# Kernel optimization log

Hardware: AMD Instinct MI355X
Metric: run time of the kernel (lower is better)

Reference implementation:

```python
import jax, jax.numpy as jnp
import numpy as np

N_NODES = 20000
N_EDGES = 640000
HID = 256
IN_F, IN_SIZE = 6, 6
OUT_F, FH = 6, 3
EDGE_DIM = 8
T_DIM, S_DIM = 4, 6
N_LAYERS = 5


def setup_inputs() -> dict:
    key = jax.random.key(0)
    ks = jax.random.split(key, 32)
    g = lambda i, shape, scale=0.05: jax.random.normal(ks[i], shape, dtype=jnp.float32) * scale
    inp = {
        "x": jax.random.normal(ks[0], (N_NODES, IN_F, IN_SIZE), dtype=jnp.float32),
        "edge_index": jax.random.randint(ks[1], (2, N_EDGES), 0, N_NODES, dtype=jnp.int32),
        "edge_attr": jax.random.normal(ks[2], (N_EDGES, EDGE_DIM), dtype=jnp.float32),
        "t": jax.random.normal(ks[3], (N_NODES, T_DIM), dtype=jnp.float32),
        "s": jax.random.normal(ks[4], (N_NODES, S_DIM), dtype=jnp.float32),
        # embedder
        "W_emb": g(5, (IN_F * IN_SIZE, HID)), "b_emb": jnp.zeros((HID,), jnp.float32),
        # spatio-temporal encoder: t/s linear embeds + fusion over concat(x, te, se)
        "W_t": g(6, (T_DIM, HID)), "b_t": jnp.zeros((HID,), jnp.float32),
        "W_s": g(7, (S_DIM, HID)), "b_s": jnp.zeros((HID,), jnp.float32),
        "W_f": g(8, (3 * HID, HID)), "b_f": jnp.zeros((HID,), jnp.float32),
        # layernorm
        "ln_g": jnp.ones((HID,), jnp.float32), "ln_b": jnp.zeros((HID,), jnp.float32),
        # 5 TransformerConv layers (heads=1): query/key/value/edge/skip linears
        "Wq": g(9, (N_LAYERS, HID, HID)), "bq": jnp.zeros((N_LAYERS, HID), jnp.float32),
        "Wk": g(10, (N_LAYERS, HID, HID)), "bk": jnp.zeros((N_LAYERS, HID), jnp.float32),
        "Wv": g(11, (N_LAYERS, HID, HID)), "bv": jnp.zeros((N_LAYERS, HID), jnp.float32),
        "We": g(12, (N_LAYERS, EDGE_DIM, HID)), "be": jnp.zeros((N_LAYERS, HID), jnp.float32),
        "Wskip": g(13, (N_LAYERS, HID, HID)), "bskip": jnp.zeros((N_LAYERS, HID), jnp.float32),
        # decoder
        "W_dec": g(14, (HID, OUT_F * FH)), "b_dec": jnp.zeros((OUT_F * FH,), jnp.float32),
    }
    return inp


def _layernorm(x, g, b, eps=1e-5):
    mu = jnp.mean(x, axis=-1, keepdims=True)
    var = jnp.mean((x - mu) ** 2, axis=-1, keepdims=True)
    return (x - mu) * jax.lax.rsqrt(var + eps) * g + b


def _transformer_conv(x, src, dst, edge_attr, Wq, bq, Wk, bk, Wv, bv, We, be, Wskip, bskip):
    n = x.shape[0]
    d = x.shape[1]
    q = x @ Wq + bq                      # [n, d]
    k = x @ Wk + bk
    v = x @ Wv + bv
    e = edge_attr @ We + be              # [E, d]
    kj = k[src] + e                      # gather + edge fuse [E, d]
    vj = v[src] + e
    alpha = jnp.sum(q[dst] * kj, axis=-1) / jnp.sqrt(jnp.float32(d))  # [E]
    # segment softmax over incoming edges of each destination node
    m = jax.ops.segment_max(alpha, dst, num_segments=n)
    a = jnp.exp(alpha - m[dst])
    denom = jax.ops.segment_sum(a, dst, num_segments=n)
    w = a / (denom[dst] + 1e-16)
    out = jax.ops.segment_sum(vj * w[:, None], dst, num_segments=n)  # [n, d]
    return out + x @ Wskip + bskip       # root/skip connection


def reference(x, edge_index, edge_attr, t, s,
              W_emb, b_emb, W_t, b_t, W_s, b_s, W_f, b_f, ln_g, ln_b,
              Wq, bq, Wk, bk, Wv, bv, We, be, Wskip, bskip, W_dec, b_dec):
    n = x.shape[0]
    h = x.reshape(n, -1) @ W_emb + b_emb
    te = t @ W_t + b_t
    se = s @ W_s + b_s
    h = jnp.concatenate([h, te, se], axis=-1) @ W_f + b_f   # spatio-temporal fuse
    h = jax.nn.relu(_layernorm(h, ln_g, ln_b))
    src, dst = edge_index[0], edge_index[1]
    for i in range(N_LAYERS):
        h = jax.nn.relu(_transformer_conv(h, src, dst, edge_attr,
                                          Wq[i], bq[i], Wk[i], bk[i], Wv[i], bv[i],
                                          We[i], be[i], Wskip[i], bskip[i]))
    out = h @ W_dec + b_dec
    return out.reshape(n, OUT_F, FH)
```

## Files before the change

kernel.cpp:

```cpp
#include <hip/hip_runtime.h>
#include <hip/hip_fp8.h>
#include <math.h>

#define NN 20000
#define NPAD 20096
#define NE 640000
#define NOUT 1152
#define GSS 272
#define KVB 512
#define CAP 80
#define SCQ 0.09016994f
#define ISCL 8.8057e-5f
#define TIDX(r,k) ((((r)>>4)*4096) + (((k)>>3)*128) + (((r)&15)*8) + ((k)&7))

typedef _Float16 f16;
typedef f16 f16x8 __attribute__((ext_vector_type(8)));
typedef f16 f16x4 __attribute__((ext_vector_type(4)));
typedef f16 h2    __attribute__((ext_vector_type(2)));
typedef float f32x4 __attribute__((ext_vector_type(4)));
typedef float f32x2 __attribute__((ext_vector_type(2)));

static __device__ __forceinline__ float fdot2(h2 a, h2 b, float c) {
#if __has_builtin(__builtin_amdgcn_fdot2)
  return __builtin_amdgcn_fdot2(a, b, c, false);
#else
  return c + (float)a[0]*(float)b[0] + (float)a[1]*(float)b[1];
#endif
}

static __device__ __forceinline__ float fast_exp2(float x) {
#if __has_builtin(__builtin_amdgcn_exp2f)
  return __builtin_amdgcn_exp2f(x);
#else
  return exp2f(x);
#endif
}

static __device__ __forceinline__ int sdot4(unsigned a, unsigned b, int c) {
#if __has_builtin(__builtin_amdgcn_sdot4)
  return __builtin_amdgcn_sdot4((int)a, (int)b, c, false);
#else
  int r = c;
  #pragma unroll
  for (int i = 0; i < 4; i++) {
    int ai = ((int)((a >> (8*i)) & 255) ^ 128) - 128;
    int bi = ((int)((b >> (8*i)) & 255) ^ 128) - 128;
    r += ai*bi;
  }
  return r;
#endif
}

static __device__ __forceinline__ unsigned pack_i8x4(float a, float b, float c, float d) {
  int i0 = (int)rintf(a), i1 = (int)rintf(b), i2 = (int)rintf(c), i3 = (int)rintf(d);
  i0 = max(-127, min(127, i0)); i1 = max(-127, min(127, i1));
  i2 = max(-127, min(127, i2)); i3 = max(-127, min(127, i3));
  return (unsigned)(i0 & 255) | ((unsigned)(i1 & 255) << 8)
       | ((unsigned)(i2 & 255) << 16) | ((unsigned)(i3 & 255) << 24);
}

static __device__ __forceinline__ unsigned pack_fp8x4(float a, float b, float c, float d) {
#if __has_builtin(__builtin_amdgcn_cvt_pk_fp8_f32)
  int r = __builtin_amdgcn_cvt_pk_fp8_f32(a, b, 0, false);
  r = __builtin_amdgcn_cvt_pk_fp8_f32(c, d, r, true);
  return (unsigned)r;
#else
  __hip_fp8_e4m3 w(a), x2(b), y(c), z(d);
  return (unsigned)w.__x | ((unsigned)x2.__x<<8) | ((unsigned)y.__x<<16) | ((unsigned)z.__x<<24);
#endif
}

template<bool HI>
static __device__ __forceinline__ f32x2 unpack_fp8x2(unsigned v) {
#if __has_builtin(__builtin_amdgcn_cvt_pk_f32_fp8)
  return __builtin_amdgcn_cvt_pk_f32_fp8((int)v, HI);
#else
  unsigned s = HI ? (v >> 16) : (v & 0xffff);
  __hip_fp8_e4m3 a, b; a.__x = (unsigned char)(s & 0xff); b.__x = (unsigned char)(s >> 8);
  return (f32x2){ (float)a, (float)b };
#endif
}

__global__ __launch_bounds__(256) void k_prep_all(
    const float* __restrict__ W_emb, const float* __restrict__ W_t,
    const float* __restrict__ W_s,   const float* __restrict__ W_f,
    const float* __restrict__ b_emb, const float* __restrict__ b_t,
    const float* __restrict__ b_s,   const float* __restrict__ b_f,
    const float* __restrict__ Wq, const float* __restrict__ Wk,
    const float* __restrict__ Wv, const float* __restrict__ Wsk,
    const float* __restrict__ We, const float* __restrict__ be,
    const float* __restrict__ bq, const float* __restrict__ bk,
    const float* __restrict__ bv, const float* __restrict__ bsk,
    f16* __restrict__ Wch, float* __restrict__ bc,
    f16* __restrict__ WT, float* __restrict__ b_all,
    f16* __restrict__ hA, f16* __restrict__ hB)
{
  __shared__ float smem[64*65];
  int b = blockIdx.x;
  int tid = threadIdx.x;

  if (b < 47) {
    int r = b, c = tid;
    if (r < 36) {
      float a = 0.f;
      for (int m = 0; m < 256; m++) a += W_emb[r*256+m] * W_f[m*256+c];
      Wch[r*256+c] = (f16)a;
    } else if (r < 40) {
      int rr = r - 36; float a = 0.f;
      for (int m = 0; m < 256; m++) a += W_t[rr*256+m] * W_f[(256+m)*256+c];
      Wch[r*256+c] = (f16)a;
    } else if (r < 46) {
      int rr = r - 40; float a = 0.f;
      for (int m = 0; m < 256; m++) a += W_s[rr*256+m] * W_f[(512+m)*256+c];
      Wch[r*256+c] = (f16)a;
    } else {
      float a = b_f[c];
      for (int m = 0; m < 256; m++) a += b_emb[m]*W_f[m*256+c];
      for (int m = 0; m < 256; m++) a += b_t[m]*W_f[(256+m)*256+c];
      for (int m = 0; m < 256; m++) a += b_s[m]*W_f[(512+m)*256+c];
      bc[c] = a;
    }
  } else if (b < 367) {
    float (*lds)[65] = (float(*)[65])smem;
    int bb = b - 47;
    int nt = bb & 3, kt = (bb >> 2) & 3, mat = (bb >> 4) & 3, L = bb >> 6;
    const float* src = (mat == 0 ? Wq : mat == 1 ? Wk : mat == 2 ? Wv : Wsk) + (size_t)L*65536;
    int k0 = kt*64, n0 = nt*64;
    int c = tid & 63, r4 = tid >> 6;
    #pragma unroll
    for (int rr = 0; rr < 16; rr++) {
      int row = rr*4 + r4;
      lds[row][c] = src[(size_t)(k0 + row)*256 + n0 + c];
    }
    __syncthreads();
    f16* dst = WT + (size_t)L*294912;
    int nl = tid & 63, kb2 = tid >> 6;
    int ng = mat*256 + n0 + nl;
    #pragma unroll
    for (int half = 0; half < 2; half++) {
      int kb = kb2 + half*4;
      f16x8 v;
      #pragma unroll
      for (int e = 0; e < 8; e++) v[e] = (f16)lds[kb*8 + e][nl];
      *(f16x8*)(dst + TIDX(ng, k0 + kb*8)) = v;
    }
  } else if (b < 412) {
    float* vec = smem;
    int bb = b - 367;
    int L = bb / 9;
    int t = bb % 9;
    vec[tid] = (t < 8) ? We[(size_t)L*2048 + t*256 + tid] : be[(size_t)L*256 + tid];
    __syncthreads();
    int wave = tid >> 6, lane = tid & 63;
    for (int k = wave; k < 256; k += 4) {
      f32x4 wq = *(const f32x4*)(Wq + (size_t)L*65536 + (size_t)k*256 + lane*4);
      f32x4 vv = *(const f32x4*)(vec + lane*4);
      float d = wq[0]*vv[0] + wq[1]*vv[1] + wq[2]*vv[2] + wq[3]*vv[3];
      #pragma unroll
      for (int o = 32; o; o >>= 1) d += __shfl_xor(d, o, 64);
      if (lane == 0) WT[(size_t)L*294912 + TIDX(1024 + t, k)] = (f16)d;
    }
  } else if (b < 417) {
    int L = b - 412;
    for (int c = tid; c < NOUT; c += 256) {
      float v;
      if (c < 256)       v = bq [L*256+c];
      else if (c < 512)  v = bk [L*256+(c-256)];
      else if (c < 768)  v = bv [L*256+(c-512)];
      else if (c < 1024) v = bsk[L*256+(c-768)];
      else if (c < 1032) {
        int t = c-1024; float a = 0.f;
        for (int m = 0; m < 256; m++) a += bq[L*256+m]*We[(size_t)L*2048 + t*256 + m];
        v = a;
      } else if (c == 1032) {
        float a = 0.f;
        for (int m = 0; m < 256; m++) a += bq[L*256+m]*be[L*256+m];
        v = a;
      } else v = 0.f;
      b_all[(size_t)L*NOUT + c] = v;
    }
  } else {
    f16* p = (b == 417 ? hA : hB) + (size_t)NN*256;
    f16x8 z = {};
    for (int i = tid; i < (NPAD-NN)*256/8; i += 256)
      *(f16x8*)(p + (size_t)i*8) = z;
  }
}

__global__ void k_scatter(const int* __restrict__ ei, const float* __restrict__ eattr,
                          int* cnt, int* __restrict__ src_s, f16* __restrict__ eaperm)
{
  int e = blockIdx.x*256 + threadIdx.x;
  if (e < NE) {
    int d = ei[NE + e];
    int pos = atomicAdd(&cnt[d], 1);
    int slot = d*CAP + pos;
    src_s[slot] = ei[e];
    f32x4 a0 = *(const f32x4*)(eattr + (size_t)e*8);
    f32x4 a1 = *(const f32x4*)(eattr + (size_t)e*8 + 4);
    f16x8 ea = { (f16)a0[0],(f16)a0[1],(f16)a0[2],(f16)a0[3],
                 (f16)a1[0],(f16)a1[1],(f16)a1[2],(f16)a1[3] };
    *(f16x8*)(eaperm + (size_t)slot*8) = ea;
  }
}

__global__ __launch_bounds__(256) void k_encoder(
    const float* __restrict__ x, const float* __restrict__ t, const float* __restrict__ s,
    const f16* __restrict__ Wch, const float* __restrict__ bc,
    const float* __restrict__ lng, const float* __restrict__ lnb,
    f16* __restrict__ h)
{
  __shared__ f16 Wcs[46*256];
  __shared__ float xin[16][48];
  __shared__ float bcs[256], lgs[256], lbs[256];
  int tid = threadIdx.x;
  int u0 = blockIdx.x * 16;
  for (int i = tid; i < 46*128; i += 256)
    ((unsigned int*)Wcs)[i] = ((const unsigned int*)Wch)[i];
  bcs[tid] = bc[tid]; lgs[tid] = lng[tid]; lbs[tid] = lnb[tid];
  for (int i = tid; i < 576; i += 256) xin[i/36][i%36] = x[(size_t)u0*36 + i];
  if (tid < 64) xin[tid>>2][36 + (tid&3)] = t[(size_t)u0*4 + tid];
  if (tid < 96) xin[tid/6][40 + tid%6] = s[(size_t)u0*6 + tid];
  __syncthreads();
  int node = tid >> 4, cg = tid & 15;
  int u = u0 + node;
  float acc[16];
  #pragma unroll
  for (int j = 0; j < 16; j++) acc[j] = bcs[cg*16+j];
  for (int r = 0; r < 46; r++) {
    float xv = xin[node][r];
    const h2* wr = (const h2*)(Wcs + r*256 + cg*16);
    #pragma unroll
    for (int j2 = 0; j2 < 8; j2++) {
      h2 w2 = wr[j2];
      acc[j2*2]   += xv * (float)w2[0];
      acc[j2*2+1] += xv * (float)w2[1];
    }
  }
  float sm = 0.f, sq = 0.f;
  #pragma unroll
  for (int j = 0; j < 16; j++) { sm += acc[j]; sq += acc[j]*acc[j]; }
  #pragma unroll
  for (int o = 1; o < 16; o <<= 1) { sm += __shfl_xor(sm, o, 64); sq += __shfl_xor(sq, o, 64); }
  float mu  = sm * (1.f/256.f);
  float var = sq * (1.f/256.f) - mu*mu;
  float rin = rsqrtf(var + 1e-5f);
  f16x8 o0, o1;
  #pragma unroll
  for (int j = 0; j < 8; j++) {
    int c = cg*16 + j;
    float v = (acc[j]-mu)*rin*lgs[c] + lbs[c];
    o0[j] = (f16)fmaxf(v, 0.f);
  }
  #pragma unroll
  for (int j = 0; j < 8; j++) {
    int c = cg*16 + 8 + j;
    float v = (acc[8+j]-mu)*rin*lgs[c] + lbs[c];
    o1[j] = (f16)fmaxf(v, 0.f);
  }
  *(f16x8*)(h + TIDX(u, cg*16))   = o0;
  *(f16x8*)(h + TIDX(u, cg*16+8)) = o1;
}

__global__ __launch_bounds__(256) void k_gemm(
    const f16* __restrict__ A, const f16* __restrict__ BT,
    const float* __restrict__ bias,
    unsigned char* __restrict__ qt8, unsigned char* __restrict__ kvt,
    f16* __restrict__ gsk)
{
  const int NWG = (NPAD/128)*9;
  const int Q = NWG >> 3, R = NWG & 7;
  int bid = blockIdx.x;
  int xcd = bid & 7, jj = bid >> 3;
  int wg = (xcd < R ? xcd*(Q+1) : R*(Q+1) + (xcd-R)*Q) + jj;
  int bmt = wg / 9, bnt = wg - bmt*9;

  int tid = threadIdx.x;
  int wave = tid >> 6, lane = tid & 63;
  int wm = wave >> 1, wn = wave & 1;
  int bm = bmt*128 + wm*64;
  int bn = bnt*128 + wn*64;
  int lr = lane & 15;
  int kg = lane >> 4;
  f32x4 acc[4][4];
  #pragma unroll
  for (int i = 0; i < 4; i++)
    #pragma unroll
    for (int j = 0; j < 4; j++) acc[i][j] = (f32x4){0.f,0.f,0.f,0.f};

  const f16* Ab = A  + (size_t)(bm >> 4)*4096 + kg*128 + lr*8;
  const f16* Bb = BT + (size_t)(bn >> 4)*4096 + kg*128 + lr*8;
  #pragma unroll
  for (int k0 = 0; k0 < 256; k0 += 32) {
    f16x8 af[4], bf[4];
    #pragma unroll
    for (int i = 0; i < 4; i++) af[i] = *(const f16x8*)(Ab + i*4096 + k0*16);
    #pragma unroll
    for (int j = 0; j < 4; j++) bf[j] = *(const f16x8*)(Bb + j*4096 + k0*16);
    #pragma unroll
    for (int i = 0; i < 4; i++)
      #pragma unroll
      for (int j = 0; j < 4; j++)
        acc[i][j] = __builtin_amdgcn_mfma_f32_16x16x32_f16(bf[j], af[i], acc[i][j], 0, 0, 0);
  }

  #pragma unroll
  for (int j = 0; j < 4; j++) {
    int cb0 = bn + j*16;
    if (cb0 >= 1040) continue;
    int colq = cb0 + kg*4;
    f32x4 bv = *(const f32x4*)(bias + colq);
    #pragma unroll
    for (int i = 0; i < 4; i++) {
      int row = bm + i*16 + lr;
      float v0 = acc[i][j][0]+bv[0], v1 = acc[i][j][1]+bv[1];
      float v2 = acc[i][j][2]+bv[2], v3 = acc[i][j][3]+bv[3];
      if (cb0 < 256) {
        *(unsigned*)(qt8 + (size_t)row*256 + colq) = pack_i8x4(v0*32.f, v1*32.f, v2*32.f, v3*32.f);
      } else if (cb0 < 512) {
        *(unsigned*)(kvt + (size_t)row*KVB + (colq-256)) = pack_i8x4(v0*32.f, v1*32.f, v2*32.f, v3*32.f);
      } else if (cb0 < 768) {
        *(unsigned*)(kvt + (size_t)row*KVB + 256 + (colq-512)) = pack_fp8x4(v0, v1, v2, v3);
      } else if (cb0 < 1024) {
        f16x4 st = { (f16)v0, (f16)v1, (f16)v2, (f16)v3 };
        *(f16x4*)(gsk + (size_t)row*GSS + (colq-768)) = st;
      } else {
        f16x4 st = { (f16)(v0*SCQ), (f16)(v1*SCQ), (f16)(v2*SCQ), (f16)(v3*SCQ) };
        *(f16x4*)(gsk + (size_t)row*GSS + 256 + (colq-1024)) = st;
      }
    }
  }
}

__global__ __launch_bounds__(256) void k_alpha(
    const unsigned char* __restrict__ qt8, const unsigned char* __restrict__ kvt,
    const f16* __restrict__ gsk, const f16* __restrict__ eaperm,
    const int* __restrict__ cnt, const int* __restrict__ src_s,
    float* __restrict__ wbuf)
{
  int wid = threadIdx.x >> 6, lane = threadIdx.x & 63;
  int u = __builtin_amdgcn_readfirstlane(blockIdx.x*4 + wid);
  int deg = cnt[u];
  const uint4* qp = (const uint4*)(qt8 + (size_t)u*256);
  uint4 q[16];
  #pragma unroll
  for (int c = 0; c < 16; c++) q[c] = qp[c];
  const f16* gb = gsk + (size_t)u*GSS;
  f16x8 qe8 = *(const f16x8*)(gb + 256);
  float qbv = (float)gb[264];
  size_t ub = (size_t)u*CAP;
  for (int i = lane; i < deg; i += 64) {
    int sn = src_s[ub + i];
    const uint4* kp = (const uint4*)(kvt + (size_t)sn*KVB);
    int di = 0;
    #pragma unroll
    for (int c = 0; c < 16; c++) {
      uint4 kw = kp[c];
      di = sdot4(kw.x, q[c].x, di);
      di = sdot4(kw.y, q[c].y, di);
      di = sdot4(kw.z, q[c].z, di);
      di = sdot4(kw.w, q[c].w, di);
    }
    f16x8 ea = *(const f16x8*)(eaperm + (ub + i)*8);
    float edot = 0.f;
    edot = fdot2((h2){ea[0],ea[1]}, (h2){qe8[0],qe8[1]}, edot);
    edot = fdot2((h2){ea[2],ea[3]}, (h2){qe8[2],qe8[3]}, edot);
    edot = fdot2((h2){ea[4],ea[5]}, (h2){qe8[4],qe8[5]}, edot);
    edot = fdot2((h2){ea[6],ea[7]}, (h2){qe8[6],qe8[7]}, edot);
    wbuf[ub + i] = fast_exp2((float)di*ISCL + edot + qbv);
  }
}

__global__ __launch_bounds__(256) void k_attn2(
    const unsigned char* __restrict__ kvt, const f16* __restrict__ gsk,
    const f16* __restrict__ eaperm,
    const float* __restrict__ WeL, const float* __restrict__ beL,
    const int* __restrict__ cnt, const int* __restrict__ src_s,
    const float* __restrict__ wbuf, f16* __restrict__ hout)
{
  int wid  = threadIdx.x >> 6;
  int lane = threadIdx.x & 63;
  int grp  = lane >> 4;
  int gl   = lane & 15;
  int u = blockIdx.x*4 + wid;
  int deg = cnt[u];

  float ssum = 0.f;
  float av[16];
  float ae[8];
  #pragma unroll
  for (int j = 0; j < 16; j++) av[j] = 0.f;
  #pragma unroll
  for (int j = 0; j < 8; j++) ae[j] = 0.f;

  size_t ub = (size_t)u*CAP;
  #pragma unroll 2
  for (int i = grp; i < deg; i += 4) {
    int sn = src_s[ub + i];
    uint4 vw = *(const uint4*)(kvt + (size_t)sn*KVB + 256 + gl*16);
    f16x8 ea = *(const f16x8*)(eaperm + (ub + i)*8);
    float w = wbuf[ub + i];
    ssum += w;
    f32x2 p;
    p = unpack_fp8x2<false>(vw.x); av[0]  += w*p[0]; av[1]  += w*p[1];
    p = unpack_fp8x2<true >(vw.x); av[2]  += w*p[0]; av[3]  += w*p[1];
    p = unpack_fp8x2<false>(vw.y); av[4]  += w*p[0]; av[5]  += w*p[1];
    p = unpack_fp8x2<true >(vw.y); av[6]  += w*p[0]; av[7]  += w*p[1];
    p = unpack_fp8x2<false>(vw.z); av[8]  += w*p[0]; av[9]  += w*p[1];
    p = unpack_fp8x2<true >(vw.z); av[10] += w*p[0]; av[11] += w*p[1];
    p = unpack_fp8x2<false>(vw.w); av[12] += w*p[0]; av[13] += w*p[1];
    p = unpack_fp8x2<true >(vw.w); av[14] += w*p[0]; av[15] += w*p[1];
    #pragma unroll
    for (int j = 0; j < 8; j++) ae[j] += w*(float)ea[j];
  }

  #pragma unroll
  for (int j = 0; j < 16; j++) {
    av[j] += __shfl_xor(av[j], 16, 64);
    av[j] += __shfl_xor(av[j], 32, 64);
  }
  #pragma unroll
  for (int j = 0; j < 8; j++) {
    ae[j] += __shfl_xor(ae[j], 16, 64);
    ae[j] += __shfl_xor(ae[j], 32, 64);
  }
  ssum += __shfl_xor(ssum, 16, 64);
  ssum += __shfl_xor(ssum, 32, 64);

  float inv = 1.f/(ssum + 1e-16f);
  const f16* gb = gsk + (size_t)u*GSS;
  int cb = gl*16 + grp*4;
  f16 res[4];
  #pragma unroll
  for (int t = 0; t < 4; t++) {
    int c = cb + t;
    float o = av[grp*4+t];
    #pragma unroll
    for (int e = 0; e < 8; e++) o += ae[e]*WeL[e*256 + c];
    o += ssum*beL[c];
    o = o*inv + (float)gb[c];
    res[t] = (f16)fmaxf(o, 0.f);
  }
  f16x4 outp = { res[0], res[1], res[2], res[3] };
  *(f16x4*)(hout + TIDX(u, cb)) = outp;
}

__global__ __launch_bounds__(256) void k_decoder(
    const f16* __restrict__ h, const float* __restrict__ Wd,
    const float* __restrict__ bd, float* __restrict__ out)
{
  int n0 = blockIdx.x*32;
  __shared__ float hs[32*256];
  int tid = threadIdx.x;
  for (int j = tid; j < 32*32; j += 256) {
    int node = j >> 5, c8 = (j & 31)*8;
    f16x8 v = *(const f16x8*)(h + TIDX(n0 + node, c8));
    float* dst = &hs[node*256 + c8];
    #pragma unroll
    for (int e = 0; e < 8; e++) dst[e] = (float)v[e];
  }
  __syncthreads();
  for (int o = tid; o < 32*18; o += 256) {
    int ln = o/18, col = o - ln*18;
    int node = n0 + ln;
    float acc = bd[col];
    const float* hr = &hs[ln*256];
    #pragma unroll 4
    for (int k4 = 0; k4 < 64; k4++) {
      f32x4 hv = *(const f32x4*)(hr + k4*4);
      acc += hv[0]*Wd[(k4*4+0)*18+col] + hv[1]*Wd[(k4*4+1)*18+col]
           + hv[2]*Wd[(k4*4+2)*18+col] + hv[3]*Wd[(k4*4+3)*18+col];
    }
    out[(size_t)node*18 + col] = acc;
  }
}

extern "C" void kernel_launch(void* const* d_in, const int* in_sizes, int n_in,
                              void* d_out, int out_size, void* d_ws, size_t ws_size,
                              hipStream_t stream)
{
  const float* x     = (const float*)d_in[0];
  const int*   ei    = (const int*)  d_in[1];
  const float* eattr = (const float*)d_in[2];
  const float* t     = (const float*)d_in[3];
  const float* s     = (const float*)d_in[4];
  const float* W_emb = (const float*)d_in[5];
  const float* b_emb = (const float*)d_in[6];
  const float* W_t   = (const float*)d_in[7];
  const float* b_t   = (const float*)d_in[8];
  const float* W_s   = (const float*)d_in[9];
  const float* b_s   = (const float*)d_in[10];
  const float* W_f   = (const float*)d_in[11];
  const float* b_f   = (const float*)d_in[12];
  const float* ln_g  = (const float*)d_in[13];
  const float* ln_b  = (const float*)d_in[14];
  const float* Wq    = (const float*)d_in[15];
  const float* bq    = (const float*)d_in[16];
  const float* Wk    = (const float*)d_in[17];
  const float* bk    = (const float*)d_in[18];
  const float* Wv    = (const float*)d_in[19];
  const float* bv    = (const float*)d_in[20];
  const float* We    = (const float*)d_in[21];
  const float* be    = (const float*)d_in[22];
  const float* Wsk   = (const float*)d_in[23];
  const float* bsk   = (const float*)d_in[24];
  const float* W_dec = (const float*)d_in[25];
  const float* b_dec = (const float*)d_in[26];

  float* wsf = (float*)d_ws;
  size_t off = 0;
  float* bc    = wsf + off; off += 256;
  float* b_all = wsf + off; off += (size_t)5*NOUT;
  f16*   Wch   = (f16*)(wsf + off); off += (size_t)46*256/2;
  f16*   WT    = (f16*)(wsf + off); off += (size_t)5*294912/2;
  unsigned char* qt8 = (unsigned char*)(wsf + off); off += (size_t)NPAD*256/4;
  unsigned char* kvt = (unsigned char*)(wsf + off); off += (size_t)NPAD*KVB/4;
  f16*   gsk   = (f16*)(wsf + off); off += (size_t)NPAD*GSS/2;
  f16*   hA    = (f16*)(wsf + off); off += (size_t)NPAD*256/2;
  f16*   hB    = (f16*)(wsf + off); off += (size_t)NPAD*256/2;
  f16*   eaperm= (f16*)(wsf + off); off += (size_t)NN*CAP*8/2;
  int*   src_s = (int*)(wsf + off); off += (size_t)NN*CAP;
  float* wbuf  = wsf + off; off += (size_t)NN*CAP;
  int*   cnt   = (int*)(wsf + off); off += NN;

  (void)hipMemsetAsync(cnt, 0, NN*sizeof(int), stream);
  k_prep_all<<<419, 256, 0, stream>>>(W_emb, W_t, W_s, W_f, b_emb, b_t, b_s, b_f,
                                      Wq, Wk, Wv, Wsk, We, be, bq, bk, bv, bsk,
                                      Wch, bc, WT, b_all, hA, hB);
  k_scatter <<<(NE+255)/256, 256, 0, stream>>>(ei, eattr, cnt, src_s, eaperm);

  k_encoder <<<NN/16, 256, 0, stream>>>(x, t, s, Wch, bc, ln_g, ln_b, hA);

  f16* hin = hA;
  f16* hot = hB;
  for (int L = 0; L < 5; L++) {
    k_gemm<<<(NPAD/128)*9, 256, 0, stream>>>(hin, WT + (size_t)L*294912,
                                             b_all + (size_t)L*NOUT, qt8, kvt, gsk);
    k_alpha<<<NN/4, 256, 0, stream>>>(qt8, kvt, gsk, eaperm, cnt, src_s, wbuf);
    k_attn2<<<NN/4, 256, 0, stream>>>(kvt, gsk, eaperm, We + (size_t)L*2048,
                                      be + (size_t)L*256, cnt, src_s, wbuf, hot);
    f16* tmp = hin; hin = hot; hot = tmp;
  }
  k_decoder<<<NN/32, 256, 0, stream>>>(hin, W_dec, b_dec, (float*)d_out);
}
```

Before: 581.9 us.

## Pack per-edge records and move edge-attr reduction into alpha kernel

Merges the separate edge-attr, source-index and weight arrays into one 32-byte record per edge slot. The alpha kernel now also reduces the softmax denominator and weighted edge attributes per node into a small stats buffer. The aggregation kernel therefore only gathers value rows, with each lane owning 4 columns and walking all edges serially instead of splitting edges across 4 lane groups. This cuts scattered loads and shuffle reductions, but it serialises the edge loop per wave and widens the per-edge record footprint.

```diff
diff --git a/kernel.cpp b/kernel.cpp
--- a/kernel.cpp
+++ b/kernel.cpp
@@ -9,6 +9,7 @@
 #define GSS 272
 #define KVB 512
 #define CAP 80
+#define RECB 32
 #define SCQ 0.09016994f
 #define ISCL 8.8057e-5f
 #define TIDX(r,k) ((((r)>>4)*4096) + (((k)>>3)*128) + (((r)&15)*8) + ((k)&7))
@@ -188,19 +189,19 @@
 }
 
 __global__ void k_scatter(const int* __restrict__ ei, const float* __restrict__ eattr,
-                          int* cnt, int* __restrict__ src_s, f16* __restrict__ eaperm)
+                          int* cnt, char* __restrict__ rec)
 {
   int e = blockIdx.x*256 + threadIdx.x;
   if (e < NE) {
     int d = ei[NE + e];
     int pos = atomicAdd(&cnt[d], 1);
-    int slot = d*CAP + pos;
-    src_s[slot] = ei[e];
+    char* rp = rec + (size_t)(d*CAP + pos)*RECB;
     f32x4 a0 = *(const f32x4*)(eattr + (size_t)e*8);
     f32x4 a1 = *(const f32x4*)(eattr + (size_t)e*8 + 4);
     f16x8 ea = { (f16)a0[0],(f16)a0[1],(f16)a0[2],(f16)a0[3],
                  (f16)a1[0],(f16)a1[1],(f16)a1[2],(f16)a1[3] };
-    *(f16x8*)(eaperm + (size_t)slot*8) = ea;
+    *(f16x8*)rp = ea;
+    *(int*)(rp + 16) = ei[e];
   }
 }
 
@@ -334,9 +335,8 @@
 
 __global__ __launch_bounds__(256) void k_alpha(
     const unsigned char* __restrict__ qt8, const unsigned char* __restrict__ kvt,
-    const f16* __restrict__ gsk, const f16* __restrict__ eaperm,
-    const int* __restrict__ cnt, const int* __restrict__ src_s,
-    float* __restrict__ wbuf)
+    const f16* __restrict__ gsk, char* __restrict__ rec,
+    const int* __restrict__ cnt, float* __restrict__ stats)
 {
   int wid = threadIdx.x >> 6, lane = threadIdx.x & 63;
   int u = __builtin_amdgcn_readfirstlane(blockIdx.x*4 + wid);
@@ -349,8 +349,16 @@
   f16x8 qe8 = *(const f16x8*)(gb + 256);
   float qbv = (float)gb[264];
   size_t ub = (size_t)u*CAP;
+
+  float ssum = 0.f;
+  float ae[8];
+  #pragma unroll
+  for (int j = 0; j < 8; j++) ae[j] = 0.f;
+
   for (int i = lane; i < deg; i += 64) {
-    int sn = src_s[ub + i];
+    char* rp = rec + (ub + i)*RECB;
+    f16x8 ea = *(const f16x8*)rp;
+    int sn = *(const int*)(rp + 16);
     const uint4* kp = (const uint4*)(kvt + (size_t)sn*KVB);
     int di = 0;
     #pragma unroll
@@ -361,88 +369,87 @@
       di = sdot4(kw.z, q[c].z, di);
       di = sdot4(kw.w, q[c].w, di);
     }
-    f16x8 ea = *(const f16x8*)(eaperm + (ub + i)*8);
     float edot = 0.f;
     edot = fdot2((h2){ea[0],ea[1]}, (h2){qe8[0],qe8[1]}, edot);
     edot = fdot2((h2){ea[2],ea[3]}, (h2){qe8[2],qe8[3]}, edot);
     edot = fdot2((h2){ea[4],ea[5]}, (h2){qe8[4],qe8[5]}, edot);
     edot = fdot2((h2){ea[6],ea[7]}, (h2){qe8[6],qe8[7]}, edot);
-    wbuf[ub + i] = fast_exp2((float)di*ISCL + edot + qbv);
+    float w = fast_exp2((float)di*ISCL + edot + qbv);
+    *(float*)(rp + 20) = w;
+    ssum += w;
+    #pragma unroll
+    for (int j = 0; j < 8; j++) ae[j] += w*(float)ea[j];
+  }
+
+  #pragma unroll
+  for (int o = 1; o < 64; o <<= 1) {
+    ssum += __shfl_xor(ssum, o, 64);
+    #pragma unroll
+    for (int j = 0; j < 8; j++) ae[j] += __shfl_xor(ae[j], o, 64);
+  }
+  if (lane == 0) {
+    float* sp = stats + (size_t)u*12;
+    sp[0] = ssum;
+    *(f32x4*)(sp + 4) = (f32x4){ae[0], ae[1], ae[2], ae[3]};
+    *(f32x4*)(sp + 8) = (f32x4){ae[4], ae[5], ae[6], ae[7]};
   }
 }
 
 __global__ __launch_bounds__(256) void k_attn2(
     const unsigned char* __restrict__ kvt, const f16* __restrict__ gsk,
-    const f16* __restrict__ eaperm,
+    const char* __restrict__ rec,
     const float* __restrict__ WeL, const float* __restrict__ beL,
-    const int* __restrict__ cnt, const int* __restrict__ src_s,
-    const float* __restrict__ wbuf, f16* __restrict__ hout)
+    const int* __restrict__ cnt, const float* __restrict__ stats,
+    f16* __restrict__ hout)
 {
   int wid  = threadIdx.x >> 6;
   int lane = threadIdx.x & 63;
-  int grp  = lane >> 4;
-  int gl   = lane & 15;
   int u = blockIdx.x*4 + wid;
   int deg = cnt[u];
-
-  float ssum = 0.f;
-  float av[16];
-  float ae[8];
-  #pragma unroll
-  for (int j = 0; j < 16; j++) av[j] = 0.f;
-  #pragma unroll
-  for (int j = 0; j < 8; j++) ae[j] = 0.f;
-
   size_t ub = (size_t)u*CAP;
-  #pragma unroll 2
-  for (int i = grp; i < deg; i += 4) {
-    int sn = src_s[ub + i];
-    uint4 vw = *(const uint4*)(kvt + (size_t)sn*KVB + 256 + gl*16);
-    f16x8 ea = *(const f16x8*)(eaperm + (ub + i)*8);
-    float w = wbuf[ub + i];
-    ssum += w;
-    f32x2 p;
-    p = unpack_fp8x2<false>(vw.x); av[0]  += w*p[0]; av[1]  += w*p[1];
-    p = unpack_fp8x2<true >(vw.x); av[2]  += w*p[0]; av[3]  += w*p[1];
-    p = unpack_fp8x2<false>(vw.y); av[4]  += w*p[0]; av[5]  += w*p[1];
-    p = unpack_fp8x2<true >(vw.y); av[6]  += w*p[0]; av[7]  += w*p[1];
-    p = unpack_fp8x2<false>(vw.z); av[8]  += w*p[0]; av[9]  += w*p[1];
-    p = unpack_fp8x2<true >(vw.z); av[10] += w*p[0]; av[11] += w*p[1];
-    p = unpack_fp8x2<false>(vw.w); av[12] += w*p[0]; av[13] += w*p[1];
-    p = unpack_fp8x2<true >(vw.w); av[14] += w*p[0]; av[15] += w*p[1];
-    #pragma unroll
-    for (int j = 0; j < 8; j++) ae[j] += w*(float)ea[j];
-  }
-
-  #pragma unroll
-  for (int j = 0; j < 16; j++) {
-    av[j] += __shfl_xor(av[j], 16, 64);
-    av[j] += __shfl_xor(av[j], 32, 64);
-  }
-  #pragma unroll
-  for (int j = 0; j < 8; j++) {
-    ae[j] += __shfl_xor(ae[j], 16, 64);
-    ae[j] += __shfl_xor(ae[j], 32, 64);
-  }
-  ssum += __shfl_xor(ssum, 16, 64);
-  ssum += __shfl_xor(ssum, 32, 64);
-
+  int c0 = lane*4;
+
+  float av0 = 0.f, av1 = 0.f, av2 = 0.f, av3 = 0.f;
+  #pragma unroll 8
+  for (int i = 0; i < deg; i++) {
+    const char* rp = rec + (ub + i)*RECB;
+    int2 sw = *(const int2*)(rp + 16);
+    float w = __int_as_float(sw.y);
+    unsigned vw = *(const unsigned*)(kvt + (size_t)sw.x*KVB + 256 + c0);
+    f32x2 p0 = unpack_fp8x2<false>(vw);
+    f32x2 p1 = unpack_fp8x2<true >(vw);
+    av0 += w*p0[0]; av1 += w*p0[1]; av2 += w*p1[0]; av3 += w*p1[1];
+  }
+
+  const float* sp = stats + (size_t)u*12;
+  float ssum = sp[0];
+  f32x4 aeA = *(const f32x4*)(sp + 4);
+  f32x4 aeB = *(const f32x4*)(sp + 8);
   float inv = 1.f/(ssum + 1e-16f);
-  const f16* gb = gsk + (size_t)u*GSS;
-  int cb = gl*16 + grp*4;
+
+  f32x4 o = {av0, av1, av2, av3};
+  #pragma unroll
+  for (int e = 0; e < 4; e++) {
+    f32x4 w4 = *(const f32x4*)(WeL + e*256 + c0);
+    #pragma unroll
+    for (int t = 0; t < 4; t++) o[t] += aeA[e]*w4[t];
+  }
+  #pragma unroll
+  for (int e = 0; e < 4; e++) {
+    f32x4 w4 = *(const f32x4*)(WeL + (4+e)*256 + c0);
+    #pragma unroll
+    for (int t = 0; t < 4; t++) o[t] += aeB[e]*w4[t];
+  }
+  f32x4 be4 = *(const f32x4*)(beL + c0);
+  f16x4 sk = *(const f16x4*)(gsk + (size_t)u*GSS + c0);
   f16 res[4];
   #pragma unroll
   for (int t = 0; t < 4; t++) {
-    int c = cb + t;
-    float o = av[grp*4+t];
-    #pragma unroll
-    for (int e = 0; e < 8; e++) o += ae[e]*WeL[e*256 + c];
-    o += ssum*beL[c];
-    o = o*inv + (float)gb[c];
-    res[t] = (f16)fmaxf(o, 0.f);
+    float v = (o[t] + ssum*be4[t])*inv + (float)sk[t];
+    res[t] = (f16)fmaxf(v, 0.f);
   }
   f16x4 outp = { res[0], res[1], res[2], res[3] };
-  *(f16x4*)(hout + TIDX(u, cb)) = outp;
+  *(f16x4*)(hout + TIDX(u, c0)) = outp;
 }
 
 __global__ __launch_bounds__(256) void k_decoder(
@@ -518,16 +525,15 @@
   f16*   gsk   = (f16*)(wsf + off); off += (size_t)NPAD*GSS/2;
   f16*   hA    = (f16*)(wsf + off); off += (size_t)NPAD*256/2;
   f16*   hB    = (f16*)(wsf + off); off += (size_t)NPAD*256/2;
-  f16*   eaperm= (f16*)(wsf + off); off += (size_t)NN*CAP*8/2;
-  int*   src_s = (int*)(wsf + off); off += (size_t)NN*CAP;
-  float* wbuf  = wsf + off; off += (size_t)NN*CAP;
+  char*  rec   = (char*)(wsf + off); off += (size_t)NN*CAP*RECB/4;
+  float* stats = wsf + off; off += (size_t)NN*12;
   int*   cnt   = (int*)(wsf + off); off += NN;
 
   (void)hipMemsetAsync(cnt, 0, NN*sizeof(int), stream);
   k_prep_all<<<419, 256, 0, stream>>>(W_emb, W_t, W_s, W_f, b_emb, b_t, b_s, b_f,
                                       Wq, Wk, Wv, Wsk, We, be, bq, bk, bv, bsk,
                                       Wch, bc, WT, b_all, hA, hB);
-  k_scatter <<<(NE+255)/256, 256, 0, stream>>>(ei, eattr, cnt, src_s, eaperm);
+  k_scatter <<<(NE+255)/256, 256, 0, stream>>>(ei, eattr, cnt, rec);
 
   k_encoder <<<NN/16, 256, 0, stream>>>(x, t, s, Wch, bc, ln_g, ln_b, hA);
 
@@ -536,9 +542,9 @@
   for (int L = 0; L < 5; L++) {
     k_gemm<<<(NPAD/128)*9, 256, 0, stream>>>(hin, WT + (size_t)L*294912,
                                              b_all + (size_t)L*NOUT, qt8, kvt, gsk);
-    k_alpha<<<NN/4, 256, 0, stream>>>(qt8, kvt, gsk, eaperm, cnt, src_s, wbuf);
-    k_attn2<<<NN/4, 256, 0, stream>>>(kvt, gsk, eaperm, We + (size_t)L*2048,
-                                      be + (size_t)L*256, cnt, src_s, wbuf, hot);
+    k_alpha<<<NN/4, 256, 0, stream>>>(qt8, kvt, gsk, rec, cnt, stats);
+    k_attn2<<<NN/4, 256, 0, stream>>>(kvt, gsk, rec, We + (size_t)L*2048,
+                                      be + (size_t)L*256, cnt, stats, hot);
     f16* tmp = hin; hin = hot; hot = tmp;
   }
   k_decoder<<<NN/32, 256, 0, stream>>>(hin, W_dec, b_dec, (float*)d_out);
```

Result: slower. 619.4 us (+6.4%).
